# Performance work log

Hardware: AMD Instinct MI355X
Metric: run time of the kernel (lower is better)

The kernel has to match this reference:

```python
import jax, jax.numpy as jnp
import numpy as np

NUM_HEADS = 8
FOCUSING_FACTOR = 3.0
EPS = 1e-6


def setup_inputs() -> dict:
    key = jax.random.key(0)
    ks = jax.random.split(key, 5)
    B, C, H, W = 16, 256, 64, 64
    hd = C // NUM_HEADS
    return {
        "x": jax.random.normal(ks[0], (B, C, H, W), jnp.float32),
        "qkv_w": jax.random.normal(ks[1], (3 * C, C), jnp.float32) * 0.02,
        "qkv_b": jnp.zeros((3 * C,), jnp.float32),
        "proj_w": jax.random.normal(ks[2], (C, C), jnp.float32) * 0.02,
        "proj_b": jnp.zeros((C,), jnp.float32),
        "dwc_w": jax.random.normal(ks[3], (hd, 1, 5, 5), jnp.float32) * 0.02,
        "dwc_b": jnp.zeros((hd,), jnp.float32),
        "scale": jnp.zeros((1, 1, C), jnp.float32),
    }


def reference(x, qkv_w, qkv_b, proj_w, proj_b, dwc_w, dwc_b, scale):
    B, C, H, W = x.shape
    N = H * W
    hd = C // NUM_HEADS

    # b c h w -> b (h w) c
    xf = x.reshape(B, C, N).transpose(0, 2, 1)
    qkv = xf @ qkv_w.T + qkv_b  # [B, N, 3C]
    q, k, v = jnp.split(qkv, 3, axis=-1)

    # focusing feature map
    q = jax.nn.relu(q) + EPS
    k = jax.nn.relu(k) + EPS
    sc = jax.nn.softplus(scale)
    q = q / sc
    k = k / sc
    q_norm = jnp.linalg.norm(q, axis=-1, keepdims=True)
    k_norm = jnp.linalg.norm(k, axis=-1, keepdims=True)
    # focusing_factor <= 6 branch
    q = q ** FOCUSING_FACTOR
    k = k ** FOCUSING_FACTOR
    q = q / jnp.linalg.norm(q, axis=-1, keepdims=True) * q_norm
    k = k / jnp.linalg.norm(k, axis=-1, keepdims=True) * k_norm

    # b n (h c) -> (b h) n c
    def to_heads(t):
        return t.reshape(B, N, NUM_HEADS, hd).transpose(0, 2, 1, 3).reshape(B * NUM_HEADS, N, hd)

    q, k, v = to_heads(q), to_heads(k), to_heads(v)

    i, j, c, d = N, N, hd, hd
    z = 1.0 / (jnp.einsum('bic,bc->bi', q, k.sum(axis=1)) + EPS)
    if i * j * (c + d) > c * d * (i + j):
        kv = jnp.einsum('bjc,bjd->bcd', k, v)  # [(BH), c, d]
        out = jnp.einsum('bic,bcd,bi->bid', q, kv, z)
    else:
        qk = jnp.einsum('bic,bjc->bij', q, k)
        out = jnp.einsum('bij,bjd,bi->bid', qk, v, z)

    # depthwise conv on v: b (w h) c -> b c w h (square map)
    num = int(N ** 0.5)
    fm = v.transpose(0, 2, 1).reshape(B * NUM_HEADS, hd, num, num)
    fm = jax.lax.conv_general_dilated(
        fm, dwc_w, window_strides=(1, 1), padding='SAME',
        feature_group_count=hd,
        dimension_numbers=('NCHW', 'OIHW', 'NCHW')) + dwc_b[None, :, None, None]
    fm = fm.reshape(B * NUM_HEADS, hd, N).transpose(0, 2, 1)
    out = out + fm

    # (b h) n c -> b n (h c)
    out = out.reshape(B, NUM_HEADS, N, hd).transpose(0, 2, 1, 3).reshape(B, N, C)
    out = out @ proj_w.T + proj_b
    # b (h w) c -> b c h w
    return out.transpose(0, 2, 1).reshape(B, C, H, W)
```

## Files before the change

kernel.cpp:

```cpp
#include <hip/hip_runtime.h>
#include <cmath>

#define B_   16
#define C_   256
#define HW_  64
#define N_   4096
#define NH_  8
#define HD_  32
#define M_   (B_ * N_)
#define QKVC (3 * C_)
#define EPS_ 1e-6f

typedef short bf16x8 __attribute__((ext_vector_type(8)));
typedef float f32x4 __attribute__((ext_vector_type(4)));
typedef unsigned int u32x4 __attribute__((ext_vector_type(4)));

__device__ __forceinline__ float b2f(unsigned short u) {
  union { unsigned int i; float f; } v;
  v.i = ((unsigned int)u) << 16;
  return v.f;
}
__device__ __forceinline__ float blo(unsigned int u) {
  union { unsigned int i; float f; } v; v.i = u << 16; return v.f;
}
__device__ __forceinline__ float bhi(unsigned int u) {
  union { unsigned int i; float f; } v; v.i = u & 0xffff0000u; return v.f;
}
__device__ __forceinline__ unsigned short f2b(float f) {
  union { float f; unsigned int i; } v;
  v.f = f;
  unsigned int r = v.i + 0x7FFFu + ((v.i >> 16) & 1u);
  return (unsigned short)(r >> 16);
}
__device__ __forceinline__ void gload_lds16(const void* g, void* l) {
  __builtin_amdgcn_global_load_lds(
      (const __attribute__((address_space(1))) void*)g,
      (__attribute__((address_space(3))) void*)l, 16, 0, 0);
}

__global__ __launch_bounds__(256) void k_cast_x(const float* __restrict__ x,
                                                unsigned short* __restrict__ xT) {
  __shared__ float t[32][33];
  const int n0 = blockIdx.x * 32, c0 = blockIdx.y * 32, b = blockIdx.z;
  const int tid = threadIdx.x;
  const int r = tid >> 3, g = (tid & 7) * 4;
  float4 v = *reinterpret_cast<const float4*>(
      &x[((size_t)(b * C_ + c0 + r)) * N_ + n0 + g]);
  t[r][g + 0] = v.x; t[r][g + 1] = v.y; t[r][g + 2] = v.z; t[r][g + 3] = v.w;
  __syncthreads();
  ushort4 o;
  o.x = f2b(t[g + 0][r]); o.y = f2b(t[g + 1][r]);
  o.z = f2b(t[g + 2][r]); o.w = f2b(t[g + 3][r]);
  *reinterpret_cast<ushort4*>(&xT[((size_t)(b * N_ + n0 + r)) * C_ + c0 + g]) = o;
}

__global__ __launch_bounds__(256) void k_cast_w(const float* __restrict__ w1,
                                                const float* __restrict__ w2,
                                                unsigned short* __restrict__ dst) {
  const int g4 = (blockIdx.x * 256 + threadIdx.x) * 4;
  float4 v;
  if (g4 < 196608) v = *reinterpret_cast<const float4*>(w1 + g4);
  else             v = *reinterpret_cast<const float4*>(w2 + (g4 - 196608));
  ushort4 o;
  o.x = f2b(v.x); o.y = f2b(v.y); o.z = f2b(v.z); o.w = f2b(v.w);
  *reinterpret_cast<ushort4*>(dst + g4) = o;
}

__global__ void k_prep_scale(const float* __restrict__ scale,
                             float* __restrict__ rsc) {
  const int c = threadIdx.x;
  rsc[c] = 1.f / log1pf(expf(scale[c]));
}

template <int LDA, int OUTMODE, int NCOL>
__global__ __launch_bounds__(256) void k_gemm(
    const unsigned short* __restrict__ A, const unsigned short* __restrict__ W,
    const float* __restrict__ bias, void* __restrict__ outp) {
  __shared__ unsigned short As[128 * 64];
  __shared__ unsigned short Bs[128 * 64];
  const int tid = threadIdx.x;
  const int wid = tid >> 6, lane = tid & 63;
  const int lin = blockIdx.x + blockIdx.y * 512;
  const int bandp = lin >> 3;
  const int rowb = bandp / NCOL;
  const int colb = bandp - rowb * NCOL;
  const int m0 = (((lin & 7) << 6) + rowb) * 128;
  const int col0 = colb * 128;
  const int wr = wid >> 1, wc = wid & 1;

  const int lrow = lane >> 3;
  const int sl = (lane & 7) ^ (lrow & 7);

  f32x4 acc[4][4];
#pragma unroll
  for (int i = 0; i < 4; ++i)
#pragma unroll
    for (int j = 0; j < 4; ++j) acc[i][j] = (f32x4){0.f, 0.f, 0.f, 0.f};

  for (int kt = 0; kt < 4; ++kt) {
    const int k0 = kt * 64;
#pragma unroll
    for (int q = 0; q < 4; ++q) {
      const int chunk = wid * 4 + q;
      const int row = chunk * 8 + lrow;
      gload_lds16(A + (size_t)(m0 + row) * LDA + k0 + sl * 8, &As[chunk * 512]);
      gload_lds16(W + (size_t)(col0 + row) * 256 + k0 + sl * 8, &Bs[chunk * 512]);
    }
    __syncthreads();

    bf16x8 fa[2][4], fb[2][4];
#pragma unroll
    for (int i = 0; i < 4; ++i) {
      const int ra = wr * 64 + i * 16 + (lane & 15);
      const int rb = wc * 64 + i * 16 + (lane & 15);
#pragma unroll
      for (int ks = 0; ks < 2; ++ks) {
        const int s = ks * 4 + (lane >> 4);
        fa[ks][i] = *reinterpret_cast<const bf16x8*>(
            &As[ra * 64 + ((s ^ (ra & 7)) * 8)]);
        fb[ks][i] = *reinterpret_cast<const bf16x8*>(
            &Bs[rb * 64 + ((s ^ (rb & 7)) * 8)]);
      }
    }
#pragma unroll
    for (int i = 0; i < 4; ++i)
#pragma unroll
      for (int j = 0; j < 4; ++j) {
        acc[i][j] = __builtin_amdgcn_mfma_f32_16x16x32_bf16(fa[0][i], fb[0][j],
                                                            acc[i][j], 0, 0, 0);
        acc[i][j] = __builtin_amdgcn_mfma_f32_16x16x32_bf16(fa[1][i], fb[1][j],
                                                            acc[i][j], 0, 0, 0);
      }
    __syncthreads();
  }

  if (OUTMODE == 0) {
    unsigned short* O = (unsigned short*)outp;
#pragma unroll
    for (int j = 0; j < 4; ++j) {
      const int colg = col0 + wc * 64 + j * 16 + (lane & 15);
      const float bb = bias[colg];
#pragma unroll
      for (int i = 0; i < 4; ++i) {
        const int mrow = m0 + wr * 64 + i * 16 + ((lane >> 4) << 2);
#pragma unroll
        for (int r = 0; r < 4; ++r)
          O[(size_t)(mrow + r) * QKVC + colg] = f2b(acc[i][j][r] + bb);
      }
    }
  } else {
    float* O = (float*)outp;
    const int b = m0 >> 12;
    const int nb0 = (m0 & 4095) + wr * 64;
#pragma unroll
    for (int j = 0; j < 4; ++j) {
      const int colg = col0 + wc * 64 + j * 16 + (lane & 15);
      const float bb = bias[colg];
#pragma unroll
      for (int i = 0; i < 4; ++i) {
        const int nb = nb0 + i * 16 + ((lane >> 4) << 2);
        f32x4 o = acc[i][j];
        o += bb;
        *reinterpret_cast<f32x4*>(&O[((size_t)(b * C_ + colg)) * N_ + nb]) = o;
      }
    }
  }
}

__global__ __launch_bounds__(256) void k_focus(unsigned short* __restrict__ qkv,
                                               const float* __restrict__ rsc) {
  const int wave = threadIdx.x >> 6, lane = threadIdx.x & 63;
  const int t = blockIdx.x * 4 + wave;
  const size_t base = (size_t)t * QKVC + lane * 4;

  uint2 qu = *reinterpret_cast<const uint2*>(qkv + base);
  uint2 ku = *reinterpret_cast<const uint2*>(qkv + base + C_);
  const f32x4 rs = *reinterpret_cast<const f32x4*>(rsc + lane * 4);

  float q[4], k[4], q3[4], k3[4];
  q[0] = blo(qu.x); q[1] = bhi(qu.x); q[2] = blo(qu.y); q[3] = bhi(qu.y);
  k[0] = blo(ku.x); k[1] = bhi(ku.x); k[2] = blo(ku.y); k[3] = bhi(ku.y);

  float sq2 = 0.f, sq6 = 0.f, sk2 = 0.f, sk6 = 0.f;
#pragma unroll
  for (int i = 0; i < 4; ++i) {
    q[i] = (fmaxf(q[i], 0.f) + EPS_) * rs[i];
    k[i] = (fmaxf(k[i], 0.f) + EPS_) * rs[i];
    const float q2 = q[i] * q[i], k2 = k[i] * k[i];
    q3[i] = q2 * q[i];
    k3[i] = k2 * k[i];
    sq2 += q2; sk2 += k2;
    sq6 += q3[i] * q3[i];
    sk6 += k3[i] * k3[i];
  }
#pragma unroll
  for (int off = 1; off < 64; off <<= 1) {
    sq2 += __shfl_xor(sq2, off);
    sq6 += __shfl_xor(sq6, off);
    sk2 += __shfl_xor(sk2, off);
    sk6 += __shfl_xor(sk6, off);
  }
  const float fq = sqrtf(sq2 / sq6);
  const float fk = sqrtf(sk2 / sk6);

  uint2 oq, ok;
  oq.x = (unsigned int)f2b(q3[0] * fq) | ((unsigned int)f2b(q3[1] * fq) << 16);
  oq.y = (unsigned int)f2b(q3[2] * fq) | ((unsigned int)f2b(q3[3] * fq) << 16);
  ok.x = (unsigned int)f2b(k3[0] * fk) | ((unsigned int)f2b(k3[1] * fk) << 16);
  ok.y = (unsigned int)f2b(k3[2] * fk) | ((unsigned int)f2b(k3[3] * fk) << 16);
  *reinterpret_cast<uint2*>(qkv + base) = oq;
  *reinterpret_cast<uint2*>(qkv + base + C_) = ok;
}

#define KVP_CHUNKS 16
__global__ __launch_bounds__(256) void k_kv_part(
    const unsigned short* __restrict__ qkv, float* __restrict__ kvp,
    float* __restrict__ ksp) {
  const int bh = blockIdx.x;
  const int chunk = blockIdx.y;
  const int b = bh >> 3, h = bh & 7;
  const int tid = threadIdx.x;
  __shared__ float ksf[64 * 36];
  __shared__ float vsf[64 * 36];

  const int c = tid >> 3;
  const int d0 = (tid & 7) * 4;
  const int srow = tid >> 2;
  const int sseg = (tid & 3) * 8;
  const int j0 = chunk * 256;

  float a0 = 0.f, a1 = 0.f, a2 = 0.f, a3 = 0.f, ksum = 0.f;

  uint4 ku, vu;
  {
    const size_t rb = ((size_t)(b * N_ + j0 + srow)) * QKVC + h * HD_ + sseg;
    ku = *reinterpret_cast<const uint4*>(qkv + rb + C_);
    vu = *reinterpret_cast<const uint4*>(qkv + rb + 2 * C_);
  }

  for (int t = 0; t < 4; ++t) {
    {
      f32x4 k0 = {blo(ku.x), bhi(ku.x), blo(ku.y), bhi(ku.y)};
      f32x4 k1 = {blo(ku.z), bhi(ku.z), blo(ku.w), bhi(ku.w)};
      f32x4 v0 = {blo(vu.x), bhi(vu.x), blo(vu.y), bhi(vu.y)};
      f32x4 v1 = {blo(vu.z), bhi(vu.z), blo(vu.w), bhi(vu.w)};
      *reinterpret_cast<f32x4*>(&ksf[srow * 36 + sseg]) = k0;
      *reinterpret_cast<f32x4*>(&ksf[srow * 36 + sseg + 4]) = k1;
      *reinterpret_cast<f32x4*>(&vsf[srow * 36 + sseg]) = v0;
      *reinterpret_cast<f32x4*>(&vsf[srow * 36 + sseg + 4]) = v1;
    }
    __syncthreads();
    if (t < 3) {
      const size_t rb =
          ((size_t)(b * N_ + j0 + (t + 1) * 64 + srow)) * QKVC + h * HD_ + sseg;
      ku = *reinterpret_cast<const uint4*>(qkv + rb + C_);
      vu = *reinterpret_cast<const uint4*>(qkv + rb + 2 * C_);
    }
#pragma unroll 8
    for (int jj = 0; jj < 64; ++jj) {
      const float kc = ksf[jj * 36 + c];
      const f32x4 vv = *reinterpret_cast<const f32x4*>(&vsf[jj * 36 + d0]);
      a0 += kc * vv[0];
      a1 += kc * vv[1];
      a2 += kc * vv[2];
      a3 += kc * vv[3];
      ksum += kc;
    }
    __syncthreads();
  }

  float* kvo = kvp + ((size_t)chunk * 128 + bh) * 1024 + c * 32 + d0;
  kvo[0] = a0; kvo[1] = a1; kvo[2] = a2; kvo[3] = a3;
  if ((tid & 7) == 0) ksp[((size_t)chunk * 128 + bh) * 32 + c] = ksum;
}

__global__ __launch_bounds__(256) void k_attn_conv_f(
    unsigned short* __restrict__ qkv, const float* __restrict__ kvp,
    const float* __restrict__ ksp, const float* __restrict__ dwc_w,
    const float* __restrict__ dwc_b) {
  const int lin = blockIdx.x;
  const int g2 = (lin & 7) * 256 + (lin >> 3);
  const int bh = g2 >> 4;
  const int ig = g2 & 15;
  const int i0 = ig * 4;
  const int b = bh >> 3, h = bh & 7;
  const int tid = threadIdx.x;
  const int wave = tid >> 6, lane = tid & 63;

  __shared__ float kv_s[1024];
  __shared__ float ksum_s[32];
  __shared__ float w_s[800];
  __shared__ float b_s[32];
  __shared__ unsigned short v_s[8 * 64 * 32];

  for (int pp = tid; pp < 1024; pp += 256) {
    float s = 0.f;
#pragma unroll
    for (int ch = 0; ch < KVP_CHUNKS; ++ch)
      s += kvp[((size_t)ch * 128 + bh) * 1024 + pp];
    kv_s[pp] = s;
  }
  if (tid < 32) {
    float s = 0.f;
#pragma unroll
    for (int ch = 0; ch < KVP_CHUNKS; ++ch)
      s += ksp[((size_t)ch * 128 + bh) * 32 + tid];
    ksum_s[tid] = s;
  }
  for (int p = tid; p < 800; p += 256)
    w_s[p] = dwc_w[(p & 31) * 25 + (p >> 5)];
  if (tid < 32) b_s[tid] = dwc_b[tid];
  __syncthreads();

#pragma unroll
  for (int rr = 0; rr < 8; ++rr) {
    const int ii = i0 + rr - 2;
    if (ii < 0 || ii >= 64) continue;
    gload_lds16(qkv + ((size_t)(b * N_ + ii * 64 + wave * 16 + (lane >> 2))) * QKVC +
                    2 * C_ + h * HD_ + (lane & 3) * 8,
                &v_s[rr * 2048 + wave * 512]);
  }

  {
    const int kb = (lane >> 4) * 8;
    const int col = lane & 15;
    bf16x8 bh0, bh1, bl0, bl1;
    float ks0[8];
#pragma unroll
    for (int t = 0; t < 8; ++t) {
      const float v0 = kv_s[(kb + t) * 32 + col];
      const float v1 = kv_s[(kb + t) * 32 + col + 16];
      const unsigned short h0 = f2b(v0), h1 = f2b(v1);
      ((unsigned short*)&bh0)[t] = h0;
      ((unsigned short*)&bh1)[t] = h1;
      ((unsigned short*)&bl0)[t] = f2b(v0 - b2f(h0));
      ((unsigned short*)&bl1)[t] = f2b(v1 - b2f(h1));
      ks0[t] = ksum_s[kb + t];
    }
    const int r0 = (i0 + wave) * 64;
#pragma unroll
    for (int rt = 0; rt < 4; ++rt) {
      const int row = r0 + rt * 16 + (lane & 15);
      const bf16x8 a = *reinterpret_cast<const bf16x8*>(
          qkv + (size_t)(b * N_ + row) * QKVC + h * HD_ + kb);
      float zp = 0.f;
#pragma unroll
      for (int t = 0; t < 8; ++t)
        zp += b2f(((const unsigned short*)&a)[t]) * ks0[t];
      zp += __shfl_xor(zp, 16);
      zp += __shfl_xor(zp, 32);
      const float z = 1.f / (zp + EPS_);

      f32x4 acc0 = {0.f, 0.f, 0.f, 0.f}, acc1 = {0.f, 0.f, 0.f, 0.f};
      acc0 = __builtin_amdgcn_mfma_f32_16x16x32_bf16(a, bl0, acc0, 0, 0, 0);
      acc1 = __builtin_amdgcn_mfma_f32_16x16x32_bf16(a, bl1, acc1, 0, 0, 0);
      acc0 = __builtin_amdgcn_mfma_f32_16x16x32_bf16(a, bh0, acc0, 0, 0, 0);
      acc1 = __builtin_amdgcn_mfma_f32_16x16x32_bf16(a, bh1, acc1, 0, 0, 0);

#pragma unroll
      for (int r = 0; r < 4; ++r) {
        const int rr = (lane >> 4) * 4 + r;
        const float zr = __shfl(z, rr);
        unsigned short* op =
            qkv + (size_t)(b * N_ + r0 + rt * 16 + rr) * QKVC + h * HD_;
        op[col] = f2b(acc0[r] * zr);
        op[col + 16] = f2b(acc1[r] * zr);
      }
    }
  }
  __syncthreads();

  {
    const int j = tid >> 2;
    const int d0 = (tid & 3) * 8;
#pragma unroll
    for (int r = 0; r < 4; ++r) {
      const int i = i0 + r;
      float fm[8];
#pragma unroll
      for (int dd = 0; dd < 8; ++dd) fm[dd] = b_s[d0 + dd];
#pragma unroll
      for (int kr = 0; kr < 5; ++kr) {
        const int ii = i + kr - 2;
        if (ii < 0 || ii >= 64) continue;
        const int lr = r + kr;
#pragma unroll
        for (int kj = 0; kj < 5; ++kj) {
          const int jj = j + kj - 2;
          if (jj < 0 || jj >= 64) continue;
          const unsigned int* vr = reinterpret_cast<const unsigned int*>(
              &v_s[lr * 2048 + jj * 32 + d0]);
          const float* wt = &w_s[(kr * 5 + kj) * 32 + d0];
#pragma unroll
          for (int p = 0; p < 4; ++p) {
            const unsigned int vu = vr[p];
            fm[2 * p + 0] += blo(vu) * wt[2 * p + 0];
            fm[2 * p + 1] += bhi(vu) * wt[2 * p + 1];
          }
        }
      }
      unsigned int* orow = reinterpret_cast<unsigned int*>(
          qkv + ((size_t)(b * N_ + i * 64 + j)) * QKVC + h * HD_ + d0);
      uint4 cur = *reinterpret_cast<const uint4*>(orow);
      unsigned int o[4] = {cur.x, cur.y, cur.z, cur.w};
#pragma unroll
      for (int p = 0; p < 4; ++p) {
        const unsigned int lo = f2b(blo(o[p]) + fm[2 * p + 0]);
        const unsigned int hi = f2b(bhi(o[p]) + fm[2 * p + 1]);
        o[p] = lo | (hi << 16);
      }
      *reinterpret_cast<uint4*>(orow) = make_uint4(o[0], o[1], o[2], o[3]);
    }
  }
}

extern "C" void kernel_launch(void* const* d_in, const int* in_sizes, int n_in,
                              void* d_out, int out_size, void* d_ws,
                              size_t ws_size, hipStream_t stream) {
  (void)in_sizes; (void)n_in; (void)out_size; (void)ws_size;
  const float* x      = (const float*)d_in[0];
  const float* qkv_w  = (const float*)d_in[1];
  const float* qkv_b  = (const float*)d_in[2];
  const float* proj_w = (const float*)d_in[3];
  const float* proj_b = (const float*)d_in[4];
  const float* dwc_w  = (const float*)d_in[5];
  const float* dwc_b  = (const float*)d_in[6];
  const float* scale  = (const float*)d_in[7];
  float* out = (float*)d_out;

  char* w = (char*)d_ws;
  unsigned short* xT   = (unsigned short*)w; w += (size_t)M_ * C_ * 2;
  unsigned short* qkvb = (unsigned short*)w; w += (size_t)M_ * QKVC * 2;
  unsigned short* wq   = (unsigned short*)w; w += (size_t)(QKVC + C_) * C_ * 2;
  unsigned short* wp   = wq + (size_t)QKVC * C_;
  float* kvp   = (float*)w;                  w += (size_t)KVP_CHUNKS * 128 * 1024 * 4;
  float* ksp   = (float*)w;                  w += (size_t)KVP_CHUNKS * 128 * 32 * 4;
  float* rscb  = (float*)w;                  w += 256 * 4;

  k_prep_scale<<<1, 256, 0, stream>>>(scale, rscb);
  k_cast_x<<<dim3(N_ / 32, C_ / 32, B_), 256, 0, stream>>>(x, xT);
  k_cast_w<<<256, 256, 0, stream>>>(qkv_w, proj_w, wq);
  k_gemm<256, 0, 6><<<dim3(512, 6), 256, 0, stream>>>(
      xT, wq, qkv_b, (void*)qkvb);
  k_focus<<<M_ / 4, 256, 0, stream>>>(qkvb, rscb);
  k_kv_part<<<dim3(128, KVP_CHUNKS), 256, 0, stream>>>(qkvb, kvp, ksp);
  k_attn_conv_f<<<2048, 256, 0, stream>>>(qkvb, kvp, ksp, dwc_w, dwc_b);
  k_gemm<768, 1, 2><<<dim3(512, 2), 256, 0, stream>>>(
      qkvb, wp, proj_b, (void*)out);
}
```

Measured before the change: 202.8 us.

## Hoist KV partial reduction into separate kernel and restructure conv loop for row reuse

Adds a small k_kv_reduce kernel that sums the per-chunk KV and k-sum partials once per head. Previously each of the 2048 attention blocks repeated that sum, 16 times per head. The depthwise conv loop is also reordered to walk the 8 input rows once, unpacking each bf16 V value once and accumulating into all 4 output rows held in registers. This cuts redundant LDS reads and bf16 conversions, but adds an extra kernel launch and raises register pressure from the 32-float accumulator array.

```diff
diff --git a/kernel.cpp b/kernel.cpp
--- a/kernel.cpp
+++ b/kernel.cpp
@@ -274,9 +274,29 @@
   if ((tid & 7) == 0) ksp[((size_t)chunk * 128 + bh) * 32 + c] = ksum;
 }
 
+__global__ __launch_bounds__(256) void k_kv_reduce(
+    const float* __restrict__ kvp, const float* __restrict__ ksp,
+    float* __restrict__ kv, float* __restrict__ ksum) {
+  const int bh = blockIdx.x;
+  for (int p = threadIdx.x; p < 1024; p += 256) {
+    float s = 0.f;
+#pragma unroll
+    for (int ch = 0; ch < KVP_CHUNKS; ++ch)
+      s += kvp[((size_t)ch * 128 + bh) * 1024 + p];
+    kv[bh * 1024 + p] = s;
+  }
+  if (threadIdx.x < 32) {
+    float s = 0.f;
+#pragma unroll
+    for (int ch = 0; ch < KVP_CHUNKS; ++ch)
+      s += ksp[((size_t)ch * 128 + bh) * 32 + threadIdx.x];
+    ksum[bh * 32 + threadIdx.x] = s;
+  }
+}
+
 __global__ __launch_bounds__(256) void k_attn_conv_f(
-    unsigned short* __restrict__ qkv, const float* __restrict__ kvp,
-    const float* __restrict__ ksp, const float* __restrict__ dwc_w,
+    unsigned short* __restrict__ qkv, const float* __restrict__ kv,
+    const float* __restrict__ ksum, const float* __restrict__ dwc_w,
     const float* __restrict__ dwc_b) {
   const int lin = blockIdx.x;
   const int g2 = (lin & 7) * 256 + (lin >> 3);
@@ -293,20 +313,8 @@
   __shared__ float b_s[32];
   __shared__ unsigned short v_s[8 * 64 * 32];
 
-  for (int pp = tid; pp < 1024; pp += 256) {
-    float s = 0.f;
-#pragma unroll
-    for (int ch = 0; ch < KVP_CHUNKS; ++ch)
-      s += kvp[((size_t)ch * 128 + bh) * 1024 + pp];
-    kv_s[pp] = s;
-  }
-  if (tid < 32) {
-    float s = 0.f;
-#pragma unroll
-    for (int ch = 0; ch < KVP_CHUNKS; ++ch)
-      s += ksp[((size_t)ch * 128 + bh) * 32 + tid];
-    ksum_s[tid] = s;
-  }
+  for (int pp = tid; pp < 1024; pp += 256) kv_s[pp] = kv[bh * 1024 + pp];
+  if (tid < 32) ksum_s[tid] = ksum[bh * 32 + tid];
   for (int p = tid; p < 800; p += 256)
     w_s[p] = dwc_w[(p & 31) * 25 + (p >> 5)];
   if (tid < 32) b_s[tid] = dwc_b[tid];
@@ -373,40 +381,51 @@
   {
     const int j = tid >> 2;
     const int d0 = (tid & 3) * 8;
+    float fm[4][8];
+#pragma unroll
+    for (int r = 0; r < 4; ++r)
+#pragma unroll
+      for (int dd = 0; dd < 8; ++dd) fm[r][dd] = b_s[d0 + dd];
+
+#pragma unroll
+    for (int lr = 0; lr < 8; ++lr) {
+      const int ii = i0 + lr - 2;
+      if (ii < 0 || ii >= 64) continue;
+#pragma unroll
+      for (int kj = 0; kj < 5; ++kj) {
+        const int jj = j + kj - 2;
+        if (jj < 0 || jj >= 64) continue;
+        const unsigned int* vr = reinterpret_cast<const unsigned int*>(
+            &v_s[lr * 2048 + jj * 32 + d0]);
+        float vf[8];
+#pragma unroll
+        for (int p = 0; p < 4; ++p) {
+          const unsigned int vu = vr[p];
+          vf[2 * p + 0] = blo(vu);
+          vf[2 * p + 1] = bhi(vu);
+        }
+#pragma unroll
+        for (int r = 0; r < 4; ++r) {
+          const int kr = lr - r;
+          if (kr < 0 || kr > 4) continue;
+          const float* wt = &w_s[(kr * 5 + kj) * 32 + d0];
+#pragma unroll
+          for (int dd = 0; dd < 8; ++dd) fm[r][dd] += vf[dd] * wt[dd];
+        }
+      }
+    }
+
 #pragma unroll
     for (int r = 0; r < 4; ++r) {
       const int i = i0 + r;
-      float fm[8];
-#pragma unroll
-      for (int dd = 0; dd < 8; ++dd) fm[dd] = b_s[d0 + dd];
-#pragma unroll
-      for (int kr = 0; kr < 5; ++kr) {
-        const int ii = i + kr - 2;
-        if (ii < 0 || ii >= 64) continue;
-        const int lr = r + kr;
-#pragma unroll
-        for (int kj = 0; kj < 5; ++kj) {
-          const int jj = j + kj - 2;
-          if (jj < 0 || jj >= 64) continue;
-          const unsigned int* vr = reinterpret_cast<const unsigned int*>(
-              &v_s[lr * 2048 + jj * 32 + d0]);
-          const float* wt = &w_s[(kr * 5 + kj) * 32 + d0];
-#pragma unroll
-          for (int p = 0; p < 4; ++p) {
-            const unsigned int vu = vr[p];
-            fm[2 * p + 0] += blo(vu) * wt[2 * p + 0];
-            fm[2 * p + 1] += bhi(vu) * wt[2 * p + 1];
-          }
-        }
-      }
       unsigned int* orow = reinterpret_cast<unsigned int*>(
           qkv + ((size_t)(b * N_ + i * 64 + j)) * QKVC + h * HD_ + d0);
       uint4 cur = *reinterpret_cast<const uint4*>(orow);
       unsigned int o[4] = {cur.x, cur.y, cur.z, cur.w};
 #pragma unroll
       for (int p = 0; p < 4; ++p) {
-        const unsigned int lo = f2b(blo(o[p]) + fm[2 * p + 0]);
-        const unsigned int hi = f2b(bhi(o[p]) + fm[2 * p + 1]);
+        const unsigned int lo = f2b(blo(o[p]) + fm[r][2 * p + 0]);
+        const unsigned int hi = f2b(bhi(o[p]) + fm[r][2 * p + 1]);
         o[p] = lo | (hi << 16);
       }
       *reinterpret_cast<uint4*>(orow) = make_uint4(o[0], o[1], o[2], o[3]);
@@ -435,6 +454,8 @@
   unsigned short* wp   = wq + (size_t)QKVC * C_;
   float* kvp   = (float*)w;                  w += (size_t)KVP_CHUNKS * 128 * 1024 * 4;
   float* ksp   = (float*)w;                  w += (size_t)KVP_CHUNKS * 128 * 32 * 4;
+  float* kvb   = (float*)w;                  w += 128 * 1024 * 4;
+  float* ksumb = (float*)w;                  w += 128 * 32 * 4;
   float* rscb  = (float*)w;                  w += 256 * 4;
 
   k_prep_scale<<<1, 256, 0, stream>>>(scale, rscb);
@@ -444,7 +465,8 @@
       xT, wq, qkv_b, (void*)qkvb);
   k_focus<<<M_ / 4, 256, 0, stream>>>(qkvb, rscb);
   k_kv_part<<<dim3(128, KVP_CHUNKS), 256, 0, stream>>>(qkvb, kvp, ksp);
-  k_attn_conv_f<<<2048, 256, 0, stream>>>(qkvb, kvp, ksp, dwc_w, dwc_b);
+  k_kv_reduce<<<128, 256, 0, stream>>>(kvp, ksp, kvb, ksumb);
+  k_attn_conv_f<<<2048, 256, 0, stream>>>(qkvb, kvb, ksumb, dwc_w, dwc_b);
   k_gemm<768, 1, 2><<<dim3(512, 2), 256, 0, stream>>>(
       qkvb, wp, proj_b, (void*)out);
 }
```

After: 195.9 us. 3.4% less time.
